# Kernel tuning notes

Measured on AMD Instinct MI355X. Metric: run time of the kernel, lower is better.

## Reference

```python
import jax, jax.numpy as jnp
import numpy as np
from math import comb

DEGREE = 10          # spline degree -> K = DEGREE+1 coefficients per pair
D = 12               # number_variables
N = 1_000_000        # sample size
SPAN = 0.1           # span_factor
# pair ordering: var_num outer loop, covar_num inner ascending -> tril row-major order
VI, CI = np.tril_indices(D, -1)
BINOM = jnp.asarray([comb(DEGREE, k) for k in range(DEGREE + 1)], dtype=jnp.float32)


def setup_inputs() -> dict:
    key = jax.random.key(0)
    k1, k2 = jax.random.split(key)
    inp = jax.random.normal(k1, (N, D), dtype=jnp.float32) * 3.0
    n_pairs = D * (D - 1) // 2  # 66
    # module inits params to 0.1 everywhere; add small noise for a non-degenerate test
    params = 0.1 + 0.05 * jax.random.normal(k2, (DEGREE + 1, n_pairs), dtype=jnp.float32)
    polynomial_range = jnp.stack([jnp.full((D,), -15.0, jnp.float32),
                                  jnp.full((D,), 15.0, jnp.float32)])
    return {"input": inp, "params": params, "polynomial_range": polynomial_range}


def _bernstein_basis(x):
    # x: [N, D] scaled to ~[0,1]; returns [N, D, K]
    i = jnp.arange(DEGREE + 1, dtype=x.dtype)
    xx = x[..., None]
    return BINOM * xx ** i * (1.0 - xx) ** (DEGREE - i)


def reference(input, params, polynomial_range):
    # inflate the polynomial range by span_factor, then scale each column to [0,1]
    low, high = polynomial_range[0], polynomial_range[1]
    width = high - low
    lo = low - SPAN * width
    hi = high + SPAN * width
    x = (input - lo) / (hi - lo)                    # [N, D]
    basis = _bernstein_basis(x)                     # [N, D, K]
    # scatter per-pair coefficients into a strictly-lower-triangular [K, D, D] tensor;
    # P[:, v, c] = params[:, pair_index(v, c)], zero elsewhere
    P = jnp.zeros((DEGREE + 1, D, D), params.dtype).at[:, VI, CI].set(params)
    # forward pass: output[n, v] = input[n, v] + sum_{c<v} lambda_{v,c}(input[n, c]) * input[n, c]
    # note lambda is multiplied by input[:, c] and lambda = basis @ coeffs, so we can fold
    # input[:, c] into the contraction only after computing lambda; here lambda*input is
    # einsum over k then elementwise — fuse: first lambda matrix entries, then weight.
    lam = jnp.einsum('nck,kvc->nvc', basis, P)      # [N, D, D] strictly lower lambda entries
    return input + jnp.einsum('nvc,nc->nv', lam, input)
```

## Files before the change

### kernel.cpp

```cpp
#include <hip/hip_runtime.h>

#define DEG 10
#define KK  11
#define DV  12
#define NP  66
#define BLK 256

__device__ __constant__ float c_binom[KK] =
    {1.f, 10.f, 45.f, 120.f, 210.f, 252.f, 210.f, 120.f, 45.f, 10.f, 1.f};

__global__ __launch_bounds__(BLK)
void decor_kernel(const float* __restrict__ in,
                  const float* __restrict__ params,
                  const float* __restrict__ pr,
                  float* __restrict__ out,
                  int n)
{
    __shared__ float sp[NP][12];
    __shared__ float sa[DV];
    __shared__ float sb[DV];

    const int tid = threadIdx.x;

    for (int i = tid; i < KK * NP; i += BLK) {
        int k = i / NP;
        int p = i - k * NP;
        sp[p][k] = params[i] * c_binom[k];
    }
    if (tid < NP) sp[tid][11] = 0.0f;
    if (tid < DV) {
        float low  = pr[tid];
        float high = pr[DV + tid];
        float w    = high - low;
        float lo   = low - 0.1f * w;
        float hi   = high + 0.1f * w;
        float inv  = 1.0f / (hi - lo);
        sa[tid] = inv;
        sb[tid] = -lo * inv;
    }
    __syncthreads();

    const int idx = blockIdx.x * BLK + tid;
    if (idx >= n) return;

    const float4* in4 = (const float4*)in;
    float4 r0 = in4[idx * 3 + 0];
    float4 r1 = in4[idx * 3 + 1];
    float4 r2 = in4[idx * 3 + 2];

    float x[DV];
    x[0] = r0.x; x[1] = r0.y; x[2]  = r0.z; x[3]  = r0.w;
    x[4] = r1.x; x[5] = r1.y; x[6]  = r1.z; x[7]  = r1.w;
    x[8] = r2.x; x[9] = r2.y; x[10] = r2.z; x[11] = r2.w;

    float acc[DV];
#pragma unroll
    for (int v = 0; v < DV; ++v) acc[v] = x[v];

#pragma unroll
    for (int c = 0; c < DV - 1; ++c) {
        float t = __builtin_fmaf(x[c], sa[c], sb[c]);
        float u = 1.0f - t;

        float b[KK];
        b[0] = 1.0f;
#pragma unroll
        for (int k = 1; k < KK; ++k) b[k] = b[k - 1] * t;
        float q = x[c];
#pragma unroll
        for (int k = KK - 1; k >= 0; --k) { b[k] *= q; q *= u; }

#pragma unroll
        for (int v = c + 1; v < DV; ++v) {
            const float* w = sp[v * (v - 1) / 2 + c];
            float4 w0 = *(const float4*)(w + 0);
            float4 w1 = *(const float4*)(w + 4);
            float4 w2 = *(const float4*)(w + 8);
            float a = acc[v];
            a = __builtin_fmaf(b[0],  w0.x, a);
            a = __builtin_fmaf(b[1],  w0.y, a);
            a = __builtin_fmaf(b[2],  w0.z, a);
            a = __builtin_fmaf(b[3],  w0.w, a);
            a = __builtin_fmaf(b[4],  w1.x, a);
            a = __builtin_fmaf(b[5],  w1.y, a);
            a = __builtin_fmaf(b[6],  w1.z, a);
            a = __builtin_fmaf(b[7],  w1.w, a);
            a = __builtin_fmaf(b[8],  w2.x, a);
            a = __builtin_fmaf(b[9],  w2.y, a);
            a = __builtin_fmaf(b[10], w2.z, a);
            acc[v] = a;
        }
    }

    float4 o0 = {acc[0], acc[1], acc[2],  acc[3]};
    float4 o1 = {acc[4], acc[5], acc[6],  acc[7]};
    float4 o2 = {acc[8], acc[9], acc[10], acc[11]};
    float4* out4 = (float4*)out;
    out4[idx * 3 + 0] = o0;
    out4[idx * 3 + 1] = o1;
    out4[idx * 3 + 2] = o2;
}

extern "C" void kernel_launch(void* const* d_in, const int* in_sizes, int n_in,
                              void* d_out, int out_size, void* d_ws, size_t ws_size,
                              hipStream_t stream)
{
    const float* in     = (const float*)d_in[0];
    const float* params = (const float*)d_in[1];
    const float* pr     = (const float*)d_in[2];
    float* out          = (float*)d_out;

    const int n = in_sizes[0] / DV;
    const int grid = (n + BLK - 1) / BLK;
    decor_kernel<<<grid, BLK, 0, stream>>>(in, params, pr, out, n);
}
```

Baseline: 132.9 us.

## Precompute scaled weights in prep kernel and read them as uniform scalar loads

Moves the per-block shared-memory setup of binomial-scaled coefficients and range affine constants into a single-block prep kernel that writes them to workspace. The main kernel then reads the weights directly from global memory with wave-uniform addresses, so the compiler can use scalar loads into SGPRs instead of LDS reads, and the per-block __syncthreads goes away. In exchange there is an extra kernel launch and a dependency on workspace size, and it relies on the compiler recognizing the loads as uniform.

```diff
diff --git a/kernel.cpp b/kernel.cpp
--- a/kernel.cpp
+++ b/kernel.cpp
@@ -6,28 +6,24 @@
 #define NP  66
 #define BLK 256
 
+#define W_OFF  0
+#define SA_OFF (NP * 12)
+#define SB_OFF (NP * 12 + DV)
+
 __device__ __constant__ float c_binom[KK] =
     {1.f, 10.f, 45.f, 120.f, 210.f, 252.f, 210.f, 120.f, 45.f, 10.f, 1.f};
 
 __global__ __launch_bounds__(BLK)
-void decor_kernel(const float* __restrict__ in,
-                  const float* __restrict__ params,
-                  const float* __restrict__ pr,
-                  float* __restrict__ out,
-                  int n)
+void prep_kernel(const float* __restrict__ params,
+                 const float* __restrict__ pr,
+                 float* __restrict__ ws)
 {
-    __shared__ float sp[NP][12];
-    __shared__ float sa[DV];
-    __shared__ float sb[DV];
-
     const int tid = threadIdx.x;
-
-    for (int i = tid; i < KK * NP; i += BLK) {
-        int k = i / NP;
-        int p = i - k * NP;
-        sp[p][k] = params[i] * c_binom[k];
+    for (int i = tid; i < NP * 12; i += BLK) {
+        const int p = i / 12;
+        const int k = i - p * 12;
+        ws[W_OFF + i] = (k < KK) ? params[k * NP + p] * c_binom[k] : 0.0f;
     }
-    if (tid < NP) sp[tid][11] = 0.0f;
     if (tid < DV) {
         float low  = pr[tid];
         float high = pr[DV + tid];
@@ -35,18 +31,24 @@
         float lo   = low - 0.1f * w;
         float hi   = high + 0.1f * w;
         float inv  = 1.0f / (hi - lo);
-        sa[tid] = inv;
-        sb[tid] = -lo * inv;
+        ws[SA_OFF + tid] = inv;
+        ws[SB_OFF + tid] = -lo * inv;
     }
-    __syncthreads();
+}
 
-    const int idx = blockIdx.x * BLK + tid;
+__global__ __launch_bounds__(BLK)
+void decor_kernel(const float* __restrict__ in,
+                  const float* __restrict__ wsp,
+                  float* __restrict__ out,
+                  int n)
+{
+    const int idx = blockIdx.x * BLK + threadIdx.x;
     if (idx >= n) return;
 
     const float4* in4 = (const float4*)in;
-    float4 r0 = in4[idx * 3 + 0];
-    float4 r1 = in4[idx * 3 + 1];
-    float4 r2 = in4[idx * 3 + 2];
+    float4 r0 = in4[(size_t)idx * 3 + 0];
+    float4 r1 = in4[(size_t)idx * 3 + 1];
+    float4 r2 = in4[(size_t)idx * 3 + 2];
 
     float x[DV];
     x[0] = r0.x; x[1] = r0.y; x[2]  = r0.z; x[3]  = r0.w;
@@ -59,7 +61,7 @@
 
 #pragma unroll
     for (int c = 0; c < DV - 1; ++c) {
-        float t = __builtin_fmaf(x[c], sa[c], sb[c]);
+        float t = __builtin_fmaf(x[c], wsp[SA_OFF + c], wsp[SB_OFF + c]);
         float u = 1.0f - t;
 
         float b[KK];
@@ -72,22 +74,19 @@
 
 #pragma unroll
         for (int v = c + 1; v < DV; ++v) {
-            const float* w = sp[v * (v - 1) / 2 + c];
-            float4 w0 = *(const float4*)(w + 0);
-            float4 w1 = *(const float4*)(w + 4);
-            float4 w2 = *(const float4*)(w + 8);
+            const float* w = wsp + W_OFF + (v * (v - 1) / 2 + c) * 12;
             float a = acc[v];
-            a = __builtin_fmaf(b[0],  w0.x, a);
-            a = __builtin_fmaf(b[1],  w0.y, a);
-            a = __builtin_fmaf(b[2],  w0.z, a);
-            a = __builtin_fmaf(b[3],  w0.w, a);
-            a = __builtin_fmaf(b[4],  w1.x, a);
-            a = __builtin_fmaf(b[5],  w1.y, a);
-            a = __builtin_fmaf(b[6],  w1.z, a);
-            a = __builtin_fmaf(b[7],  w1.w, a);
-            a = __builtin_fmaf(b[8],  w2.x, a);
-            a = __builtin_fmaf(b[9],  w2.y, a);
-            a = __builtin_fmaf(b[10], w2.z, a);
+            a = __builtin_fmaf(b[0],  w[0],  a);
+            a = __builtin_fmaf(b[1],  w[1],  a);
+            a = __builtin_fmaf(b[2],  w[2],  a);
+            a = __builtin_fmaf(b[3],  w[3],  a);
+            a = __builtin_fmaf(b[4],  w[4],  a);
+            a = __builtin_fmaf(b[5],  w[5],  a);
+            a = __builtin_fmaf(b[6],  w[6],  a);
+            a = __builtin_fmaf(b[7],  w[7],  a);
+            a = __builtin_fmaf(b[8],  w[8],  a);
+            a = __builtin_fmaf(b[9],  w[9],  a);
+            a = __builtin_fmaf(b[10], w[10], a);
             acc[v] = a;
         }
     }
@@ -96,9 +95,9 @@
     float4 o1 = {acc[4], acc[5], acc[6],  acc[7]};
     float4 o2 = {acc[8], acc[9], acc[10], acc[11]};
     float4* out4 = (float4*)out;
-    out4[idx * 3 + 0] = o0;
-    out4[idx * 3 + 1] = o1;
-    out4[idx * 3 + 2] = o2;
+    out4[(size_t)idx * 3 + 0] = o0;
+    out4[(size_t)idx * 3 + 1] = o1;
+    out4[(size_t)idx * 3 + 2] = o2;
 }
 
 extern "C" void kernel_launch(void* const* d_in, const int* in_sizes, int n_in,
@@ -109,8 +108,11 @@
     const float* params = (const float*)d_in[1];
     const float* pr     = (const float*)d_in[2];
     float* out          = (float*)d_out;
+    float* ws           = (float*)d_ws;
 
     const int n = in_sizes[0] / DV;
+
+    prep_kernel<<<1, BLK, 0, stream>>>(params, pr, ws);
     const int grid = (n + BLK - 1) / BLK;
-    decor_kernel<<<grid, BLK, 0, stream>>>(in, params, pr, out, n);
+    decor_kernel<<<grid, BLK, 0, stream>>>(in, ws, out, n);
 }
```

New measurement: 119.3 us. 10.2% less time.
